# Kernel tuning notes

Measured on AMD Instinct MI355X. Metric: run time of the kernel, lower is better.

Reference implementation:

```python
import jax, jax.numpy as jnp
import numpy as np

N = 20000      # nodes
E = 320000     # edges per timestep
T = 16         # timesteps
F_IN = 128     # node_features
F1, H1 = 64, 4 # gat1 filters/heads (concat=True)
F2, H2 = 64, 4 # gat2 filters/heads (concat=False -> mean over heads)
NEG_SLOPE = 0.2
EPS = 1e-16


def setup_inputs() -> dict:
    key = jax.random.key(0)
    ks = jax.random.split(key, 18)
    s = 0.05
    rn = lambda k, shp: (jax.random.normal(k, shp, jnp.float32) * s)
    return {
        "x_sequence": jax.random.normal(ks[0], (N, T, F_IN), jnp.float32),
        "edge_index_sequence": jax.random.randint(ks[1], (T, 2, E), 0, N, jnp.int32),
        # GATConv 1 (in=F_IN, out=F1, heads=H1, concat=True)
        "W1": rn(ks[2], (F_IN, H1 * F1)),
        "att_src1": rn(ks[3], (H1, F1)),
        "att_dst1": rn(ks[4], (H1, F1)),
        "b1": rn(ks[5], (H1 * F1,)),
        # GATConv 2 (in=H1*F1, out=F2, heads=H2, concat=False)
        "W2": rn(ks[6], (H1 * F1, H2 * F2)),
        "att_src2": rn(ks[7], (H2, F2)),
        "att_dst2": rn(ks[8], (H2, F2)),
        "b2": rn(ks[9], (F2,)),
        # GRU (input=F2, hidden=F2); layout: x @ W_ih + b_ih, gates [r|z|n]
        "W_ih": rn(ks[10], (F2, 3 * F2)),
        "W_hh": rn(ks[11], (F2, 3 * F2)),
        "b_ih": rn(ks[12], (3 * F2,)),
        "b_hh": rn(ks[13], (3 * F2,)),
        # final Linear(F2 -> 1)
        "W_out": rn(ks[14], (F2, 1)),
        "b_out": rn(ks[15], (1,)),
    }


def _gat(x, src, dst, W, a_src, a_dst, bias, heads, out_ch, concat):
    """PyG-style GATConv with self-loops already appended to (src, dst)."""
    n = x.shape[0]
    h = (x @ W).reshape(n, heads, out_ch)            # [N, H, C]
    al_src = jnp.einsum("nhc,hc->nh", h, a_src)       # [N, H]
    al_dst = jnp.einsum("nhc,hc->nh", h, a_dst)
    e = al_src[src] + al_dst[dst]                     # [E, H]
    e = jax.nn.leaky_relu(e, NEG_SLOPE)
    # segment softmax over edges grouped by destination node
    m = jax.ops.segment_max(e, dst, num_segments=n)   # [N, H]
    e = jnp.exp(e - m[dst])
    denom = jax.ops.segment_sum(e, dst, num_segments=n)
    alpha = e / (denom[dst] + EPS)                    # [E, H]
    msg = h[src] * alpha[:, :, None]                  # [E, H, C]
    out = jax.ops.segment_sum(msg, dst, num_segments=n)  # [N, H, C]
    out = out.reshape(n, heads * out_ch) if concat else out.mean(axis=1)
    return out + bias


def reference(x_sequence, edge_index_sequence, W1, att_src1, att_dst1, b1,
              W2, att_src2, att_dst2, b2, W_ih, W_hh, b_ih, b_hh, W_out, b_out):
    loops = jnp.arange(N, dtype=edge_index_sequence.dtype)

    def gat_step(_, inp):
        x_t, ei = inp                                 # [N,F_IN], [2,E]
        src = jnp.concatenate([ei[0], loops])         # add self-loops
        dst = jnp.concatenate([ei[1], loops])
        h = jax.nn.relu(_gat(x_t, src, dst, W1, att_src1, att_dst1, b1, H1, F1, True))
        h = jax.nn.relu(_gat(h, src, dst, W2, att_src2, att_dst2, b2, H2, F2, False))
        return None, h

    xs = (jnp.swapaxes(x_sequence, 0, 1), edge_index_sequence)  # [T,N,F_IN], [T,2,E]
    _, gat_out = jax.lax.scan(gat_step, None, xs)               # [T, N, F2]

    def gru_step(h_prev, x_t):
        gi = x_t @ W_ih + b_ih
        gh = h_prev @ W_hh + b_hh
        ir, iz, ig = jnp.split(gi, 3, axis=-1)
        hr, hz, hg = jnp.split(gh, 3, axis=-1)
        r = jax.nn.sigmoid(ir + hr)
        z = jax.nn.sigmoid(iz + hz)
        g = jnp.tanh(ig + r * hg)
        h = (1.0 - z) * g + z * h_prev
        return h, None

    h0 = jnp.zeros((N, F2), x_sequence.dtype)
    h_last, _ = jax.lax.scan(gru_step, h0, gat_out)             # [N, F2]
    return (h_last @ W_out + b_out).squeeze(-1)                  # [N]
```

## Files before the change

### kernel.cpp

```cpp
#include <hip/hip_runtime.h>
#include <math.h>

#define N_NODES 20000
#define N_EDGES 320000
#define T_STEPS 16
#define TB 8
#define RB_ROWS (N_NODES * TB)
#define F_INDIM 128
#define HC 256
#define HEADS 4
#define CDIM 64
#define G3 192
#define EPN (N_EDGES + N_NODES)
#define CSR_NB 10
#define CSR_EPB 32000

typedef __attribute__((ext_vector_type(8))) short bf16x8;
typedef __attribute__((ext_vector_type(8))) unsigned short ushort8;
typedef __attribute__((ext_vector_type(4))) float f32x4;
typedef __attribute__((ext_vector_type(4))) _Float16 half4;

__device__ inline unsigned short f2bf(float x) {
    unsigned int u = __builtin_bit_cast(unsigned int, x);
    u += 0x7fffu + ((u >> 16) & 1u);
    return (unsigned short)(u >> 16);
}
__device__ inline void split_hilo(float x, unsigned short& h, unsigned short& l) {
    h = f2bf(x);
    float hf = __builtin_bit_cast(float, (unsigned int)h << 16);
    l = f2bf(x - hf);
}
__device__ inline float fsig(float x) { return 1.f / (1.f + __expf(-x)); }
__device__ inline float ftanh(float x) {
    x = fminf(fmaxf(x, -15.f), 15.f);
    float e = __expf(2.f * x);
    return (e - 1.f) / (e + 1.f);
}


__global__ void k_f2bf(const float* __restrict__ in, unsigned short* __restrict__ out, int n4) {
    int i = blockIdx.x * 256 + threadIdx.x;
    if (i >= n4) return;
    float4 v = ((const float4*)in)[i];
    ushort8 o;
    split_hilo(v.x, ((unsigned short*)&o)[0], ((unsigned short*)&o)[1]);
    split_hilo(v.y, ((unsigned short*)&o)[2], ((unsigned short*)&o)[3]);
    split_hilo(v.z, ((unsigned short*)&o)[4], ((unsigned short*)&o)[5]);
    split_hilo(v.w, ((unsigned short*)&o)[6], ((unsigned short*)&o)[7]);
    ((ushort8*)out)[i] = o;
}

__global__ void k_wsplit(const float* __restrict__ W, unsigned short* __restrict__ Wt,
                         int K, int Ncol) {
    int idx = blockIdx.x * 256 + threadIdx.x;
    if (idx >= K * Ncol) return;
    int k = idx / Ncol, c = idx - k * Ncol;
    unsigned short h, l;
    split_hilo(W[idx], h, l);
    Wt[(size_t)c * 2 * K + 2 * k] = h;
    Wt[(size_t)c * 2 * K + 2 * k + 1] = l;
}


__global__ __launch_bounds__(1024) void k_csr_hist(const int* __restrict__ ei,
                                                   unsigned int* __restrict__ partial,
                                                   unsigned short* __restrict__ lrank16) {
    __shared__ unsigned int hist[N_NODES];
    const int t = blockIdx.y, b = blockIdx.x;
    const int tid = threadIdx.x;
    for (int i = tid; i < N_NODES; i += 1024) hist[i] = 0;
    __syncthreads();
    const int* dst = ei + (size_t)t * 2 * N_EDGES + N_EDGES;
    const int e1 = min(b * CSR_EPB + CSR_EPB, N_EDGES);
    for (int e = b * CSR_EPB + tid; e < e1; e += 1024) {
        unsigned int lr = atomicAdd(&hist[dst[e]], 1u);
        lrank16[(size_t)t * N_EDGES + e] = (unsigned short)lr;
    }
    __syncthreads();
    unsigned int* pp = partial + ((size_t)t * CSR_NB + b) * N_NODES;
    for (int i = tid; i < N_NODES; i += 1024) pp[i] = hist[i];
}

__global__ void k_csr_colscan(unsigned int* __restrict__ partial,
                              unsigned int* __restrict__ total) {
    int idx = blockIdx.x * 256 + threadIdx.x;
    if (idx >= T_STEPS * N_NODES) return;
    int t = idx / N_NODES;
    int d = idx - t * N_NODES;
    unsigned int* pb = partial + (size_t)t * CSR_NB * N_NODES + d;
    unsigned int acc = 0;
#pragma unroll
    for (int b = 0; b < CSR_NB; ++b) {
        unsigned int c = pb[(size_t)b * N_NODES];
        pb[(size_t)b * N_NODES] = acc;
        acc += c;
    }
    total[idx] = acc + 1;
}

__global__ __launch_bounds__(1024) void k_csr_scan(const unsigned int* __restrict__ total,
                                                   int* __restrict__ off_all,
                                                   unsigned short* __restrict__ csr16) {
    __shared__ int sdata[1024];
    const int t = blockIdx.x;
    const unsigned int* tot = total + (size_t)t * N_NODES;
    int* off = off_all + t * (N_NODES + 1);
    unsigned short* cs = csr16 + (size_t)t * EPN;
    const int tid = threadIdx.x;
    const int ITEMS = (N_NODES + 1023) / 1024;
    const int start = tid * ITEMS;
    int local = 0;
    for (int i = 0; i < ITEMS; ++i) {
        int d = start + i;
        if (d < N_NODES) local += tot[d];
    }
    sdata[tid] = local;
    __syncthreads();
    for (int s = 1; s < 1024; s <<= 1) {
        int v = (tid >= s) ? sdata[tid - s] : 0;
        __syncthreads();
        sdata[tid] += v;
        __syncthreads();
    }
    int run = sdata[tid] - local;
    for (int i = 0; i < ITEMS; ++i) {
        int d = start + i;
        if (d < N_NODES) {
            off[d] = run;
            cs[run] = (unsigned short)d;
            run += tot[d];
        }
    }
    if (tid == 0) off[N_NODES] = EPN;
}

__global__ void k_csr_fold(unsigned int* __restrict__ partial,
                           const int* __restrict__ off_all) {
    int idx = blockIdx.x * 256 + threadIdx.x;
    if (idx >= T_STEPS * CSR_NB * N_NODES) return;
    int t = idx / (CSR_NB * N_NODES);
    int rem = idx - t * (CSR_NB * N_NODES);
    int d = rem % N_NODES;
    partial[idx] += (unsigned int)(off_all[t * (N_NODES + 1) + d] + 1);
}

__global__ void k_csr_fill(const int* __restrict__ ei,
                           const unsigned int* __restrict__ partial,
                           const unsigned short* __restrict__ lrank16,
                           unsigned short* __restrict__ csr16) {
    const int bid = blockIdx.x;
    const int t = bid & 15;
    const int i = bid >> 4;
    const int e = i * 256 + threadIdx.x;
    const int* ep = ei + (size_t)t * 2 * N_EDGES;
    int s = ep[e], d = ep[N_EDGES + e];
    int b = e / CSR_EPB;
    unsigned int pos = partial[((size_t)t * CSR_NB + b) * N_NODES + d]
                     + lrank16[(size_t)t * N_EDGES + e];
    csr16[(size_t)t * EPN + pos] = (unsigned short)s;
}


template <bool XMAP, bool ATTN, bool CHALF, int BN>
__global__ __launch_bounds__(256) void k_gemm_mfma(const unsigned short* __restrict__ A, int lda,
                                                   const unsigned short* __restrict__ Bt,
                                                   float* __restrict__ C, int ldc,
                                                   int K2, int tbase,
                                                   const float* __restrict__ a_src,
                                                   const float* __restrict__ a_dst,
                                                   float* __restrict__ asb,
                                                   float* __restrict__ adb) {
    __shared__ unsigned short sA[128][40];
    __shared__ unsigned short sB[BN][40];
    const int NJ = BN / 16;
    const int tid = threadIdx.x;
    const int wid = tid >> 6, lane = tid & 63;
    const int row0 = blockIdx.y * 128;
    const int col0 = blockIdx.x * BN;

    const int ar = tid >> 1, aq = (tid & 1) * 8;
    const int bc = tid >> 2, bq = (tid & 3) * 8;

    int l = row0 + ar;
    int rg;
    if (XMAP) { int tl = l / N_NODES; int s = l - tl * N_NODES; rg = s * T_STEPS + tbase + tl; }
    else rg = l;
    const unsigned short* Arow = A + (size_t)rg * lda;
    const unsigned short* Brow = Bt + (size_t)(col0 + bc) * K2;
    const unsigned short* Brow2 = (BN == 128) ? (Bt + (size_t)(col0 + bc + 64) * K2) : Brow;

    const int fr = lane & 15;
    const int kg = lane >> 4;

    f32x4 acc[2][NJ] = {};

    for (int kk = 0; kk < K2; kk += 32) {
        ushort8 a0 = *(const ushort8*)(Arow + kk + aq);
        ushort8 a1 = *(const ushort8*)(Arow + kk + aq + 16);
        ushort8 b0 = *(const ushort8*)(Brow + kk + bq);
        ushort8 b1;
        if (BN == 128) b1 = *(const ushort8*)(Brow2 + kk + bq);
        *(ushort8*)&sA[ar][aq] = a0;
        *(ushort8*)&sA[ar][aq + 16] = a1;
        *(ushort8*)&sB[bc][bq] = b0;
        if (BN == 128) *(ushort8*)&sB[bc + 64][bq] = b1;
        __syncthreads();
        bf16x8 af[2], bfv[NJ];
#pragma unroll
        for (int i = 0; i < 2; ++i)
            af[i] = *(const bf16x8*)&sA[wid * 32 + i * 16 + fr][kg * 8];
#pragma unroll
        for (int j = 0; j < NJ; ++j)
            bfv[j] = *(const bf16x8*)&sB[j * 16 + fr][kg * 8];
#pragma unroll
        for (int i = 0; i < 2; ++i)
#pragma unroll
            for (int j = 0; j < NJ; ++j)
                acc[i][j] = __builtin_amdgcn_mfma_f32_16x16x32_bf16(af[i], bfv[j], acc[i][j],
                                                                   0, 0, 0);
        __syncthreads();
    }
#pragma unroll
    for (int i = 0; i < 2; ++i)
#pragma unroll
        for (int j = 0; j < NJ; ++j) {
            int col = col0 + j * 16 + fr;
#pragma unroll
            for (int r = 0; r < 4; ++r) {
                int row = row0 + wid * 32 + i * 16 + kg * 4 + r;
                if (CHALF) {
                    _Float16* Ch = (_Float16*)C;
                    Ch[(size_t)row * ldc + col] = (_Float16)acc[i][j][r];
                } else {
                    C[(size_t)row * ldc + col] = acc[i][j][r];
                }
            }
        }

    if (ATTN) {
#pragma unroll
        for (int half = 0; half < BN / 64; ++half) {
            const int h_idx = (col0 >> 6) + half;
            float wa[4], wb[4];
#pragma unroll
            for (int j = 0; j < 4; ++j) {
                wa[j] = a_src[h_idx * 64 + j * 16 + fr];
                wb[j] = a_dst[h_idx * 64 + j * 16 + fr];
            }
#pragma unroll
            for (int i = 0; i < 2; ++i)
#pragma unroll
                for (int r = 0; r < 4; ++r) {
                    float sa = 0.f, sd = 0.f;
#pragma unroll
                    for (int j = 0; j < 4; ++j) {
                        sa = fmaf(acc[i][half * 4 + j][r], wa[j], sa);
                        sd = fmaf(acc[i][half * 4 + j][r], wb[j], sd);
                    }
#pragma unroll
                    for (int s = 1; s <= 8; s <<= 1) {
                        sa += __shfl_xor(sa, s, 64);
                        sd += __shfl_xor(sd, s, 64);
                    }
                    if (fr == 0) {
                        int row = row0 + wid * 32 + i * 16 + kg * 4 + r;
                        asb[(size_t)row * 4 + h_idx] = sa;
                        adb[(size_t)row * 4 + h_idx] = sd;
                    }
                }
        }
    }
}


template <bool CONCAT>
__global__ __launch_bounds__(256) void k_agg(const _Float16* __restrict__ hfeat,
                                             const float* __restrict__ asb,
                                             const float* __restrict__ adb,
                                             const int* __restrict__ off_all,
                                             const unsigned short* __restrict__ csr16,
                                             const float* __restrict__ bias,
                                             unsigned short* __restrict__ out, int tbase) {
    const int bid = blockIdx.x;
    const int tl = bid & 7;
    const int nb = bid >> 3;
    const int t = tbase + tl;
    const int wid = threadIdx.x >> 6;
    const int d = nb * 4 + wid;
    const int lane = threadIdx.x & 63;
    const int h = lane >> 4;
    const int e16 = lane & 15;
    const int* off = off_all + (size_t)t * (N_NODES + 1);
    const int beg = off[d];
    const int deg = off[d + 1] - beg;
    const unsigned short* cs = csr16 + (size_t)t * EPN + beg;
    const float* asl = asb + (size_t)tl * N_NODES * HEADS;
    const half4* feat = (const half4*)(hfeat + (size_t)tl * N_NODES * HC);
    const float adh = adb[((size_t)tl * N_NODES + d) * HEADS + h];

    float ax = 0.f, ay = 0.f, az = 0.f, aw = 0.f, dlane = 0.f;
    const int widx = (lane & 48);
    for (int base = 0; base < deg; base += 16) {
        int e = base + e16;
        int sreg = 0;
        float wme = 0.f;
        if (e < deg) {
            sreg = cs[e];
            float sc = asl[sreg * 4 + h] + adh;
            sc = sc > 0.f ? sc : 0.2f * sc;
            wme = __expf(sc);
        }
        dlane += wme;
        const int len = min(16, deg - base);
        int q = 0;
        for (; q + 4 <= len; q += 4) {
#pragma unroll
            for (int u = 0; u < 4; ++u) {
                int qq = q + u;
                float wq = __shfl(wme, widx | qq, 64);
                int sq = __builtin_amdgcn_readlane(sreg, qq);
                half4 v = feat[(size_t)sq * 64 + lane];
                ax = fmaf(wq, (float)v[0], ax);
                ay = fmaf(wq, (float)v[1], ay);
                az = fmaf(wq, (float)v[2], az);
                aw = fmaf(wq, (float)v[3], aw);
            }
        }
        for (; q < len; ++q) {
            float wq = __shfl(wme, widx | q, 64);
            int sq = __builtin_amdgcn_readlane(sreg, q);
            half4 v = feat[(size_t)sq * 64 + lane];
            ax = fmaf(wq, (float)v[0], ax);
            ay = fmaf(wq, (float)v[1], ay);
            az = fmaf(wq, (float)v[2], az);
            aw = fmaf(wq, (float)v[3], aw);
        }
    }
    float denom = dlane;
#pragma unroll
    for (int s = 1; s <= 8; s <<= 1) denom += __shfl_xor(denom, s, 64);
    float inv = 1.f / (denom + 1e-16f);
    ax *= inv; ay *= inv; az *= inv; aw *= inv;

    if (CONCAT) {
        float4 b = ((const float4*)bias)[lane];
        float v0 = fmaxf(ax + b.x, 0.f), v1 = fmaxf(ay + b.y, 0.f);
        float v2 = fmaxf(az + b.z, 0.f), v3 = fmaxf(aw + b.w, 0.f);
        ushort8 o;
        split_hilo(v0, ((unsigned short*)&o)[0], ((unsigned short*)&o)[1]);
        split_hilo(v1, ((unsigned short*)&o)[2], ((unsigned short*)&o)[3]);
        split_hilo(v2, ((unsigned short*)&o)[4], ((unsigned short*)&o)[5]);
        split_hilo(v3, ((unsigned short*)&o)[6], ((unsigned short*)&o)[7]);
        *(ushort8*)(out + ((size_t)tl * N_NODES + d) * (2 * HC) + lane * 8) = o;
    } else {
        ax += __shfl_xor(ax, 16, 64); ax += __shfl_xor(ax, 32, 64);
        ay += __shfl_xor(ay, 16, 64); ay += __shfl_xor(ay, 32, 64);
        az += __shfl_xor(az, 16, 64); az += __shfl_xor(az, 32, 64);
        aw += __shfl_xor(aw, 16, 64); aw += __shfl_xor(aw, 32, 64);
        if (h == 0) {
            float4 b = ((const float4*)bias)[e16];
            float v0 = fmaxf(ax * 0.25f + b.x, 0.f), v1 = fmaxf(ay * 0.25f + b.y, 0.f);
            float v2 = fmaxf(az * 0.25f + b.z, 0.f), v3 = fmaxf(aw * 0.25f + b.w, 0.f);
            ushort8 o;
            split_hilo(v0, ((unsigned short*)&o)[0], ((unsigned short*)&o)[1]);
            split_hilo(v1, ((unsigned short*)&o)[2], ((unsigned short*)&o)[3]);
            split_hilo(v2, ((unsigned short*)&o)[4], ((unsigned short*)&o)[5]);
            split_hilo(v3, ((unsigned short*)&o)[6], ((unsigned short*)&o)[7]);
            *(ushort8*)(out + ((size_t)d * T_STEPS + t) * (2 * CDIM) + e16 * 8) = o;
        }
    }
}


#define GRU_NPB 40
#define GRU_THREADS 512

__global__ __launch_bounds__(GRU_THREADS, 4) void k_gru_all(const float* __restrict__ GI,
                                                            const float* __restrict__ Whh,
                                                            const float* __restrict__ bih,
                                                            const float* __restrict__ bhh,
                                                            const float* __restrict__ Wout,
                                                            const float* __restrict__ bout,
                                                            float* __restrict__ out) {
    __shared__ f32x4 sWp[16 * 3 * 64];
    __shared__ float sH[GRU_NPB][68];
    const int tid = threadIdx.x;
    const int c = tid & 63;
    const int ng = tid >> 6;
    const int n0 = ng * 5;
    const int nid0 = blockIdx.x * GRU_NPB + n0;

    for (int i = tid; i < 16 * 3 * 64; i += GRU_THREADS) {
        int k4 = i / 192, rem = i - k4 * 192;
        int pp = rem >> 6, cc = rem & 63;
        f32x4 w;
#pragma unroll
        for (int q = 0; q < 4; ++q) w[q] = Whh[(k4 * 4 + q) * G3 + pp * 64 + cc];
        sWp[i] = w;
    }
    for (int i = tid; i < GRU_NPB * 68; i += GRU_THREADS) ((float*)sH)[i] = 0.f;
    __syncthreads();

    const float bi0 = bih[c], bi1 = bih[64 + c], bi2 = bih[128 + c];
    const float bh0 = bhh[c], bh1 = bhh[64 + c], bh2 = bhh[128 + c];

    for (int t = 0; t < T_STEPS; ++t) {
        float gi0[5], gi1[5], gi2[5];
#pragma unroll
        for (int n = 0; n < 5; ++n) {
            const float* gp = GI + ((size_t)(nid0 + n) * T_STEPS + t) * G3;
            gi0[n] = gp[c]; gi1[n] = gp[64 + c]; gi2[n] = gp[128 + c];
        }
        float a0[5] = {}, a1[5] = {}, a2[5] = {};
#pragma unroll 4
        for (int k4 = 0; k4 < 16; ++k4) {
            f32x4 h4[5];
#pragma unroll
            for (int n = 0; n < 5; ++n) h4[n] = *(const f32x4*)&sH[n0 + n][k4 * 4];
            f32x4 w0 = sWp[(k4 * 3 + 0) * 64 + c];
            f32x4 w1 = sWp[(k4 * 3 + 1) * 64 + c];
            f32x4 w2 = sWp[(k4 * 3 + 2) * 64 + c];
#pragma unroll
            for (int q = 0; q < 4; ++q)
#pragma unroll
                for (int n = 0; n < 5; ++n) {
                    float hv = h4[n][q];
                    a0[n] = fmaf(hv, w0[q], a0[n]);
                    a1[n] = fmaf(hv, w1[q], a1[n]);
                    a2[n] = fmaf(hv, w2[q], a2[n]);
                }
        }
#pragma unroll
        for (int n = 0; n < 5; ++n) {
            float r = fsig(gi0[n] + bi0 + a0[n] + bh0);
            float z = fsig(gi1[n] + bi1 + a1[n] + bh1);
            float g = ftanh(gi2[n] + bi2 + r * (a2[n] + bh2));
            sH[n0 + n][c] = (1.f - z) * g + z * sH[n0 + n][c];
        }
    }

    float wc = Wout[c];
    float b0 = bout[0];
#pragma unroll
    for (int n = 0; n < 5; ++n) {
        float v = sH[n0 + n][c] * wc;
#pragma unroll
        for (int s = 32; s >= 1; s >>= 1) v += __shfl_xor(v, s, 64);
        if (c == 0) out[nid0 + n] = v + b0;
    }
}


extern "C" void kernel_launch(void* const* d_in, const int* in_sizes, int n_in,
                              void* d_out, int out_size, void* d_ws, size_t ws_size,
                              hipStream_t stream) {
    const float* x   = (const float*)d_in[0];
    const int*   ei  = (const int*)d_in[1];
    const float* W1  = (const float*)d_in[2];
    const float* as1 = (const float*)d_in[3];
    const float* ad1 = (const float*)d_in[4];
    const float* b1  = (const float*)d_in[5];
    const float* W2  = (const float*)d_in[6];
    const float* as2 = (const float*)d_in[7];
    const float* ad2 = (const float*)d_in[8];
    const float* b2  = (const float*)d_in[9];
    const float* Wih = (const float*)d_in[10];
    const float* Whh = (const float*)d_in[11];
    const float* bih = (const float*)d_in[12];
    const float* bhh = (const float*)d_in[13];
    const float* Wout = (const float*)d_in[14];
    const float* bout = (const float*)d_in[15];

    char* p = (char*)d_ws;
    float* h_half = (float*)p;
    float* GI_all = (float*)p;  p += 163840000;
    unsigned short* g1_bf = (unsigned short*)p;  p += 163840000;
    unsigned short* g2_bf = (unsigned short*)p;  p += 81920000;
    unsigned short* x_bf  = (unsigned short*)p;  p += 163840000;
    float* asb = (float*)p;  p += 2560000;
    float* adb = (float*)p;  p += 2560000;
    unsigned short* w1t  = (unsigned short*)p;  p += 131072;
    unsigned short* w2t  = (unsigned short*)p;  p += 262144;
    unsigned short* wiht = (unsigned short*)p;  p += 49152;
    int* off_all = (int*)p;  p += 1280064;
    unsigned short* csr16 = (unsigned short*)p;  p += 10880000;
    unsigned int* partial = (unsigned int*)p;  p += (size_t)T_STEPS * CSR_NB * N_NODES * 4;
    unsigned int* total = (unsigned int*)p;  p += (size_t)T_STEPS * N_NODES * 4;
    unsigned short* lrank16 = (unsigned short*)p;  p += (size_t)T_STEPS * N_EDGES * 2;

    dim3 thr(256);

    k_f2bf<<<(N_NODES * T_STEPS * F_INDIM / 4 + 255) / 256, thr, 0, stream>>>(
        x, x_bf, N_NODES * T_STEPS * F_INDIM / 4);
    k_wsplit<<<(F_INDIM * HC + 255) / 256, thr, 0, stream>>>(W1, w1t, F_INDIM, HC);
    k_wsplit<<<(HC * HC + 255) / 256, thr, 0, stream>>>(W2, w2t, HC, HC);
    k_wsplit<<<(CDIM * G3 + 255) / 256, thr, 0, stream>>>(Wih, wiht, CDIM, G3);

    k_csr_hist<<<dim3(CSR_NB, T_STEPS), 1024, 0, stream>>>(ei, partial, lrank16);
    k_csr_colscan<<<(T_STEPS * N_NODES + 255) / 256, thr, 0, stream>>>(partial, total);
    k_csr_scan<<<T_STEPS, 1024, 0, stream>>>(total, off_all, csr16);
    k_csr_fold<<<(T_STEPS * CSR_NB * N_NODES + 255) / 256, thr, 0, stream>>>(partial, off_all);
    k_csr_fill<<<(N_EDGES / 256) * T_STEPS, thr, 0, stream>>>(ei, partial, lrank16, csr16);

    for (int hb = 0; hb < 2; ++hb) {
        const int tbase = hb * TB;
        k_gemm_mfma<true, true, true, 128><<<dim3(2, RB_ROWS / 128), thr, 0, stream>>>(
            x_bf, 2 * F_INDIM, w1t, h_half, HC, 2 * F_INDIM, tbase, as1, ad1, asb, adb);
        k_agg<true><<<N_NODES / 4 * TB, thr, 0, stream>>>(
            (const _Float16*)h_half, asb, adb, off_all, csr16, b1, g1_bf, tbase);
        k_gemm_mfma<false, true, true, 128><<<dim3(2, RB_ROWS / 128), thr, 0, stream>>>(
            g1_bf, 2 * HC, w2t, h_half, HC, 2 * HC, tbase, as2, ad2, asb, adb);
        k_agg<false><<<N_NODES / 4 * TB, thr, 0, stream>>>(
            (const _Float16*)h_half, asb, adb, off_all, csr16, b2, g2_bf, tbase);
    }

    k_gemm_mfma<false, false, false, 64><<<dim3(3, N_NODES * T_STEPS / 128), thr, 0, stream>>>(
        g2_bf, 2 * CDIM, wiht, GI_all, G3, 2 * CDIM, 0, nullptr, nullptr, nullptr, nullptr);

    k_gru_all<<<N_NODES / GRU_NPB, GRU_THREADS, 0, stream>>>(GI_all, Whh, bih, bhh, Wout, bout,
                                                            (float*)d_out);
}
```

Measured before the change: 1.372 ms.

## Fuse input conversion into GEMM and GRU input projection into GRU kernel

Removes the separate fp32-to-bf16 hi/lo conversion pass over x by having the first GEMM load fp32 directly and split it in registers. It also drops the standalone GI GEMM: the GRU kernel now stages the g2 activations per timestep in shared memory and computes the input projection alongside the hidden projection, which avoids writing and re-reading a large GI buffer. The CSR histogram block count is doubled. The trade-off is more FMA work and shared memory in the GRU kernel, plus an extra barrier per step and lower occupancy (launch bounds drop to 1 block).

```diff
diff --git a/kernel.cpp b/kernel.cpp
--- a/kernel.cpp
+++ b/kernel.cpp
@@ -12,8 +12,8 @@
 #define CDIM 64
 #define G3 192
 #define EPN (N_EDGES + N_NODES)
-#define CSR_NB 10
-#define CSR_EPB 32000
+#define CSR_NB 20
+#define CSR_EPB 16000
 
 typedef __attribute__((ext_vector_type(8))) short bf16x8;
 typedef __attribute__((ext_vector_type(8))) unsigned short ushort8;
@@ -29,6 +29,18 @@
     h = f2bf(x);
     float hf = __builtin_bit_cast(float, (unsigned int)h << 16);
     l = f2bf(x - hf);
+}
+__device__ inline ushort8 f4_to_hilo(float4 v) {
+    ushort8 o;
+    split_hilo(v.x, ((unsigned short*)&o)[0], ((unsigned short*)&o)[1]);
+    split_hilo(v.y, ((unsigned short*)&o)[2], ((unsigned short*)&o)[3]);
+    split_hilo(v.z, ((unsigned short*)&o)[4], ((unsigned short*)&o)[5]);
+    split_hilo(v.w, ((unsigned short*)&o)[6], ((unsigned short*)&o)[7]);
+    return o;
+}
+__device__ inline float hilo_to_f(unsigned short h, unsigned short l) {
+    return __builtin_bit_cast(float, (unsigned int)h << 16) +
+           __builtin_bit_cast(float, (unsigned int)l << 16);
 }
 __device__ inline float fsig(float x) { return 1.f / (1.f + __expf(-x)); }
 __device__ inline float ftanh(float x) {
@@ -37,18 +49,6 @@
     return (e - 1.f) / (e + 1.f);
 }
 
-
-__global__ void k_f2bf(const float* __restrict__ in, unsigned short* __restrict__ out, int n4) {
-    int i = blockIdx.x * 256 + threadIdx.x;
-    if (i >= n4) return;
-    float4 v = ((const float4*)in)[i];
-    ushort8 o;
-    split_hilo(v.x, ((unsigned short*)&o)[0], ((unsigned short*)&o)[1]);
-    split_hilo(v.y, ((unsigned short*)&o)[2], ((unsigned short*)&o)[3]);
-    split_hilo(v.z, ((unsigned short*)&o)[4], ((unsigned short*)&o)[5]);
-    split_hilo(v.w, ((unsigned short*)&o)[6], ((unsigned short*)&o)[7]);
-    ((ushort8*)out)[i] = o;
-}
 
 __global__ void k_wsplit(const float* __restrict__ W, unsigned short* __restrict__ Wt,
                          int K, int Ncol) {
@@ -161,7 +161,7 @@
 }
 
 
-template <bool XMAP, bool ATTN, bool CHALF, int BN>
+template <bool XMAP, bool ATTN, bool CHALF, int BN, bool AF32>
 __global__ __launch_bounds__(256) void k_gemm_mfma(const unsigned short* __restrict__ A, int lda,
                                                    const unsigned short* __restrict__ Bt,
                                                    float* __restrict__ C, int ldc,
@@ -186,6 +186,7 @@
     if (XMAP) { int tl = l / N_NODES; int s = l - tl * N_NODES; rg = s * T_STEPS + tbase + tl; }
     else rg = l;
     const unsigned short* Arow = A + (size_t)rg * lda;
+    const float* Arowf = (const float*)A + (size_t)rg * lda;
     const unsigned short* Brow = Bt + (size_t)(col0 + bc) * K2;
     const unsigned short* Brow2 = (BN == 128) ? (Bt + (size_t)(col0 + bc + 64) * K2) : Brow;
 
@@ -195,8 +196,16 @@
     f32x4 acc[2][NJ] = {};
 
     for (int kk = 0; kk < K2; kk += 32) {
-        ushort8 a0 = *(const ushort8*)(Arow + kk + aq);
-        ushort8 a1 = *(const ushort8*)(Arow + kk + aq + 16);
+        ushort8 a0, a1;
+        if (AF32) {
+            float4 fa0 = *(const float4*)(Arowf + ((kk + aq) >> 1));
+            float4 fa1 = *(const float4*)(Arowf + ((kk + aq) >> 1) + 8);
+            a0 = f4_to_hilo(fa0);
+            a1 = f4_to_hilo(fa1);
+        } else {
+            a0 = *(const ushort8*)(Arow + kk + aq);
+            a1 = *(const ushort8*)(Arow + kk + aq + 16);
+        }
         ushort8 b0 = *(const ushort8*)(Brow + kk + bq);
         ushort8 b1;
         if (BN == 128) b1 = *(const ushort8*)(Brow2 + kk + bq);
@@ -375,28 +384,36 @@
 #define GRU_NPB 40
 #define GRU_THREADS 512
 
-__global__ __launch_bounds__(GRU_THREADS, 4) void k_gru_all(const float* __restrict__ GI,
+__global__ __launch_bounds__(GRU_THREADS, 1) void k_gru_all(const unsigned short* __restrict__ g2bf,
+                                                            const float* __restrict__ Wih,
                                                             const float* __restrict__ Whh,
                                                             const float* __restrict__ bih,
                                                             const float* __restrict__ bhh,
                                                             const float* __restrict__ Wout,
                                                             const float* __restrict__ bout,
                                                             float* __restrict__ out) {
-    __shared__ f32x4 sWp[16 * 3 * 64];
+    __shared__ f32x4 sWh[16 * 3 * 64];
+    __shared__ f32x4 sWi[16 * 3 * 64];
     __shared__ float sH[GRU_NPB][68];
+    __shared__ float sX[GRU_NPB][68];
     const int tid = threadIdx.x;
     const int c = tid & 63;
     const int ng = tid >> 6;
     const int n0 = ng * 5;
     const int nid0 = blockIdx.x * GRU_NPB + n0;
+    const int blk0 = blockIdx.x * GRU_NPB;
 
     for (int i = tid; i < 16 * 3 * 64; i += GRU_THREADS) {
         int k4 = i / 192, rem = i - k4 * 192;
         int pp = rem >> 6, cc = rem & 63;
-        f32x4 w;
-#pragma unroll
-        for (int q = 0; q < 4; ++q) w[q] = Whh[(k4 * 4 + q) * G3 + pp * 64 + cc];
-        sWp[i] = w;
+        f32x4 wh, wi;
+#pragma unroll
+        for (int q = 0; q < 4; ++q) {
+            wh[q] = Whh[(k4 * 4 + q) * G3 + pp * 64 + cc];
+            wi[q] = Wih[(k4 * 4 + q) * G3 + pp * 64 + cc];
+        }
+        sWh[i] = wh;
+        sWi[i] = wi;
     }
     for (int i = tid; i < GRU_NPB * 68; i += GRU_THREADS) ((float*)sH)[i] = 0.f;
     __syncthreads();
@@ -405,38 +422,54 @@
     const float bh0 = bhh[c], bh1 = bhh[64 + c], bh2 = bhh[128 + c];
 
     for (int t = 0; t < T_STEPS; ++t) {
-        float gi0[5], gi1[5], gi2[5];
-#pragma unroll
-        for (int n = 0; n < 5; ++n) {
-            const float* gp = GI + ((size_t)(nid0 + n) * T_STEPS + t) * G3;
-            gi0[n] = gp[c]; gi1[n] = gp[64 + c]; gi2[n] = gp[128 + c];
-        }
+        for (int idx = tid; idx < GRU_NPB * 16; idx += GRU_THREADS) {
+            int n = idx >> 4, g = idx & 15;
+            ushort8 v = *(const ushort8*)(g2bf +
+                ((size_t)(blk0 + n) * T_STEPS + t) * (2 * CDIM) + g * 8);
+#pragma unroll
+            for (int j = 0; j < 4; ++j)
+                sX[n][g * 4 + j] = hilo_to_f(((unsigned short*)&v)[2 * j],
+                                             ((unsigned short*)&v)[2 * j + 1]);
+        }
+        __syncthreads();
+
         float a0[5] = {}, a1[5] = {}, a2[5] = {};
+        float i0[5] = {}, i1[5] = {}, i2[5] = {};
 #pragma unroll 4
         for (int k4 = 0; k4 < 16; ++k4) {
-            f32x4 h4[5];
-#pragma unroll
-            for (int n = 0; n < 5; ++n) h4[n] = *(const f32x4*)&sH[n0 + n][k4 * 4];
-            f32x4 w0 = sWp[(k4 * 3 + 0) * 64 + c];
-            f32x4 w1 = sWp[(k4 * 3 + 1) * 64 + c];
-            f32x4 w2 = sWp[(k4 * 3 + 2) * 64 + c];
+            f32x4 h4[5], x4[5];
+#pragma unroll
+            for (int n = 0; n < 5; ++n) {
+                h4[n] = *(const f32x4*)&sH[n0 + n][k4 * 4];
+                x4[n] = *(const f32x4*)&sX[n0 + n][k4 * 4];
+            }
+            f32x4 wh0 = sWh[(k4 * 3 + 0) * 64 + c];
+            f32x4 wh1 = sWh[(k4 * 3 + 1) * 64 + c];
+            f32x4 wh2 = sWh[(k4 * 3 + 2) * 64 + c];
+            f32x4 wi0 = sWi[(k4 * 3 + 0) * 64 + c];
+            f32x4 wi1 = sWi[(k4 * 3 + 1) * 64 + c];
+            f32x4 wi2 = sWi[(k4 * 3 + 2) * 64 + c];
 #pragma unroll
             for (int q = 0; q < 4; ++q)
 #pragma unroll
                 for (int n = 0; n < 5; ++n) {
-                    float hv = h4[n][q];
-                    a0[n] = fmaf(hv, w0[q], a0[n]);
-                    a1[n] = fmaf(hv, w1[q], a1[n]);
-                    a2[n] = fmaf(hv, w2[q], a2[n]);
+                    float hv = h4[n][q], xv = x4[n][q];
+                    a0[n] = fmaf(hv, wh0[q], a0[n]);
+                    a1[n] = fmaf(hv, wh1[q], a1[n]);
+                    a2[n] = fmaf(hv, wh2[q], a2[n]);
+                    i0[n] = fmaf(xv, wi0[q], i0[n]);
+                    i1[n] = fmaf(xv, wi1[q], i1[n]);
+                    i2[n] = fmaf(xv, wi2[q], i2[n]);
                 }
         }
 #pragma unroll
         for (int n = 0; n < 5; ++n) {
-            float r = fsig(gi0[n] + bi0 + a0[n] + bh0);
-            float z = fsig(gi1[n] + bi1 + a1[n] + bh1);
-            float g = ftanh(gi2[n] + bi2 + r * (a2[n] + bh2));
+            float r = fsig(i0[n] + bi0 + a0[n] + bh0);
+            float z = fsig(i1[n] + bi1 + a1[n] + bh1);
+            float g = ftanh(i2[n] + bi2 + r * (a2[n] + bh2));
             sH[n0 + n][c] = (1.f - z) * g + z * sH[n0 + n][c];
         }
+        __syncthreads();
     }
 
     float wc = Wout[c];
@@ -472,16 +505,13 @@
     const float* bout = (const float*)d_in[15];
 
     char* p = (char*)d_ws;
-    float* h_half = (float*)p;
-    float* GI_all = (float*)p;  p += 163840000;
+    float* h_half = (float*)p;  p += 81920000;
     unsigned short* g1_bf = (unsigned short*)p;  p += 163840000;
     unsigned short* g2_bf = (unsigned short*)p;  p += 81920000;
-    unsigned short* x_bf  = (unsigned short*)p;  p += 163840000;
     float* asb = (float*)p;  p += 2560000;
     float* adb = (float*)p;  p += 2560000;
     unsigned short* w1t  = (unsigned short*)p;  p += 131072;
     unsigned short* w2t  = (unsigned short*)p;  p += 262144;
-    unsigned short* wiht = (unsigned short*)p;  p += 49152;
     int* off_all = (int*)p;  p += 1280064;
     unsigned short* csr16 = (unsigned short*)p;  p += 10880000;
     unsigned int* partial = (unsigned int*)p;  p += (size_t)T_STEPS * CSR_NB * N_NODES * 4;
@@ -490,11 +520,8 @@
 
     dim3 thr(256);
 
-    k_f2bf<<<(N_NODES * T_STEPS * F_INDIM / 4 + 255) / 256, thr, 0, stream>>>(
-        x, x_bf, N_NODES * T_STEPS * F_INDIM / 4);
     k_wsplit<<<(F_INDIM * HC + 255) / 256, thr, 0, stream>>>(W1, w1t, F_INDIM, HC);
     k_wsplit<<<(HC * HC + 255) / 256, thr, 0, stream>>>(W2, w2t, HC, HC);
-    k_wsplit<<<(CDIM * G3 + 255) / 256, thr, 0, stream>>>(Wih, wiht, CDIM, G3);
 
     k_csr_hist<<<dim3(CSR_NB, T_STEPS), 1024, 0, stream>>>(ei, partial, lrank16);
     k_csr_colscan<<<(T_STEPS * N_NODES + 255) / 256, thr, 0, stream>>>(partial, total);
@@ -504,19 +531,17 @@
 
     for (int hb = 0; hb < 2; ++hb) {
         const int tbase = hb * TB;
-        k_gemm_mfma<true, true, true, 128><<<dim3(2, RB_ROWS / 128), thr, 0, stream>>>(
-            x_bf, 2 * F_INDIM, w1t, h_half, HC, 2 * F_INDIM, tbase, as1, ad1, asb, adb);
+        k_gemm_mfma<true, true, true, 128, true><<<dim3(2, RB_ROWS / 128), thr, 0, stream>>>(
+            (const unsigned short*)x, F_INDIM, w1t, h_half, HC, 2 * F_INDIM, tbase,
+            as1, ad1, asb, adb);
         k_agg<true><<<N_NODES / 4 * TB, thr, 0, stream>>>(
             (const _Float16*)h_half, asb, adb, off_all, csr16, b1, g1_bf, tbase);
-        k_gemm_mfma<false, true, true, 128><<<dim3(2, RB_ROWS / 128), thr, 0, stream>>>(
+        k_gemm_mfma<false, true, true, 128, false><<<dim3(2, RB_ROWS / 128), thr, 0, stream>>>(
             g1_bf, 2 * HC, w2t, h_half, HC, 2 * HC, tbase, as2, ad2, asb, adb);
         k_agg<false><<<N_NODES / 4 * TB, thr, 0, stream>>>(
             (const _Float16*)h_half, asb, adb, off_all, csr16, b2, g2_bf, tbase);
     }
 
-    k_gemm_mfma<false, false, false, 64><<<dim3(3, N_NODES * T_STEPS / 128), thr, 0, stream>>>(
-        g2_bf, 2 * CDIM, wiht, GI_all, G3, 2 * CDIM, 0, nullptr, nullptr, nullptr, nullptr);
-
-    k_gru_all<<<N_NODES / GRU_NPB, GRU_THREADS, 0, stream>>>(GI_all, Whh, bih, bhh, Wout, bout,
-                                                            (float*)d_out);
-}
+    k_gru_all<<<N_NODES / GRU_NPB, GRU_THREADS, 0, stream>>>(g2_bf, Wih, Whh, bih, bhh,
+                                                            Wout, bout, (float*)d_out);
+}
```

Result: slower. 1.411 ms (+2.8%).
